# Kernel optimization log

Hardware: AMD Instinct MI355X
Metric: run time of the kernel (lower is better)

Reference implementation:

```python
import jax, jax.numpy as jnp
import numpy as np

B, S, D, I = 4, 2048, 4096, 11008

def setup_inputs() -> dict:
    key = jax.random.key(0)
    ks = jax.random.split(key, 7)
    x = jax.random.normal(ks[0], (B, S, D), dtype=jnp.float32)
    # int8 weights stored as int32 carriers with int8-range values
    gate_w = jax.random.randint(ks[1], (I, D), -127, 128, dtype=jnp.int32)
    up_w = jax.random.randint(ks[2], (I, D), -127, 128, dtype=jnp.int32)
    down_w = jax.random.randint(ks[3], (D, I), -127, 128, dtype=jnp.int32)
    # per-tensor scales (fp16 in original; fp32 here for a clean baseline)
    gate_s = jax.random.uniform(ks[4], (1,), dtype=jnp.float32) * 0.01 + 0.001
    up_s = jax.random.uniform(ks[5], (1,), dtype=jnp.float32) * 0.01 + 0.001
    down_s = jax.random.uniform(ks[6], (1,), dtype=jnp.float32) * 0.01 + 0.001
    return {"x": x, "gate_w": gate_w, "gate_s": gate_s,
            "up_w": up_w, "up_s": up_s, "down_w": down_w, "down_s": down_s}

def _dequant_matmul(x, w_int8, scale):
    # y = x @ (w * s)^T == (x @ w^T) * s  (per-tensor scale commutes)
    w = w_int8.astype(x.dtype)
    return jnp.einsum('bsd,od->bso', x, w) * scale

def reference(x, gate_w, gate_s, up_w, up_s, down_w, down_s):
    gate = jax.nn.silu(_dequant_matmul(x, gate_w, gate_s))  # [B,S,I]
    up = _dequant_matmul(x, up_w, up_s)                      # [B,S,I]
    out = _dequant_matmul(gate * up, down_w, down_s)         # [B,S,D]
    return out.astype(x.dtype)
```

## Files before the change

kernel.cpp:

```cpp
#include <hip/hip_runtime.h>
#include <hip/hip_fp16.h>

#define MTOK 8192
#define DDIM 4096
#define IDIM 11008

#define BM 256
#define BN 128
#define BK 64
#define NTHR 512

typedef _Float16 f16x4 __attribute__((ext_vector_type(4)));
typedef _Float16 f16x8 __attribute__((ext_vector_type(8)));
typedef float    f32x4 __attribute__((ext_vector_type(4)));

__global__ __launch_bounds__(256) void cvt_x_kernel(const float* __restrict__ src,
                                                    _Float16* __restrict__ dst, int n4) {
  int stride = gridDim.x * blockDim.x;
  for (int i = blockIdx.x * blockDim.x + threadIdx.x; i < n4; i += stride) {
    float4 v = ((const float4*)src)[i];
    f16x4 h;
    h.x = (_Float16)v.x; h.y = (_Float16)v.y; h.z = (_Float16)v.z; h.w = (_Float16)v.w;
    ((f16x4*)dst)[i] = h;
  }
}

__global__ __launch_bounds__(256) void cvt_w_kernel(const int* __restrict__ src,
                                                    _Float16* __restrict__ dst, int n4) {
  int stride = gridDim.x * blockDim.x;
  for (int i = blockIdx.x * blockDim.x + threadIdx.x; i < n4; i += stride) {
    int4 v = ((const int4*)src)[i];
    f16x4 h;
    h.x = (_Float16)v.x; h.y = (_Float16)v.y; h.z = (_Float16)v.z; h.w = (_Float16)v.w;
    ((f16x4*)dst)[i] = h;
  }
}

template<int ROWS>
__device__ __forceinline__ void stage_tile(const _Float16* __restrict__ gbase, int ldk,
                                           _Float16* stile, int tid) {
#pragma unroll
  for (int it = 0; it < (ROWS * 8) / NTHR; ++it) {
    int slot = it * NTHR + tid;
    int r = slot >> 3, c = slot & 7;
    int csrc = c ^ (r & 7);
    const _Float16* gp = gbase + (long)r * ldk + csrc * 8;
    __builtin_amdgcn_global_load_lds(
        (const __attribute__((address_space(1))) void*)gp,
        (__attribute__((address_space(3))) void*)(stile + slot * 8),
        16, 0, 0);
  }
}

__device__ __forceinline__ f16x8 frag_ld(const _Float16* s, int row, int cbase) {
  int c = cbase ^ (row & 7);
  return *(const f16x8*)(s + (row * 8 + c) * 8);
}

__global__ __launch_bounds__(NTHR, 2) void gemm_gateup(
    const _Float16* __restrict__ X, const _Float16* __restrict__ Wg,
    const _Float16* __restrict__ Wu, const float* __restrict__ gs_p,
    const float* __restrict__ us_p, _Float16* __restrict__ H) {
  constexpr int ASZ = BM * BK;
  constexpr int BSZ = BN * BK;
  constexpr int BUF = ASZ + 2 * BSZ;
  __shared__ _Float16 lds[2 * BUF] __attribute__((aligned(16)));

  int tid = threadIdx.x;
  int bm = blockIdx.x, bn = blockIdx.y;
  int lane = tid & 63, w = tid >> 6;
  int wm = (w >> 1) * 64, wn = (w & 1) * 64;
  int lr = lane & 15, q = lane >> 4;

  const _Float16* Abase = X + (long)bm * BM * DDIM;
  const _Float16* Gbase = Wg + (long)bn * BN * DDIM;
  const _Float16* Ubase = Wu + (long)bn * BN * DDIM;

  f32x4 accg[4][4], accu[4][4];
#pragma unroll
  for (int i = 0; i < 4; ++i)
#pragma unroll
    for (int j = 0; j < 4; ++j) {
      accg[i][j] = (f32x4){0.f, 0.f, 0.f, 0.f};
      accu[i][j] = (f32x4){0.f, 0.f, 0.f, 0.f};
    }

  stage_tile<BM>(Abase, DDIM, lds, tid);
  stage_tile<BN>(Gbase, DDIM, lds + ASZ, tid);
  stage_tile<BN>(Ubase, DDIM, lds + ASZ + BSZ, tid);
  asm volatile("s_waitcnt vmcnt(0)" ::: "memory");
  __builtin_amdgcn_s_barrier();

  constexpr int NT = DDIM / BK;
#pragma unroll 1
  for (int t = 0; t < NT; ++t) {
    _Float16* cb = lds + (t & 1) * BUF;
    if (t + 1 < NT) {
      _Float16* nb = lds + ((t + 1) & 1) * BUF;
      int k0 = (t + 1) * BK;
      stage_tile<BM>(Abase + k0, DDIM, nb, tid);
      stage_tile<BN>(Gbase + k0, DDIM, nb + ASZ, tid);
      stage_tile<BN>(Ubase + k0, DDIM, nb + ASZ + BSZ, tid);
    }
#pragma unroll
    for (int kk = 0; kk < 2; ++kk) {
      int cbase = kk * 4 + q;
      f16x8 a[4], bg[4], bu[4];
#pragma unroll
      for (int i = 0; i < 4; ++i) a[i] = frag_ld(cb, wm + i * 16 + lr, cbase);
#pragma unroll
      for (int j = 0; j < 4; ++j) {
        bg[j] = frag_ld(cb + ASZ, wn + j * 16 + lr, cbase);
        bu[j] = frag_ld(cb + ASZ + BSZ, wn + j * 16 + lr, cbase);
      }
#pragma unroll
      for (int i = 0; i < 4; ++i)
#pragma unroll
        for (int j = 0; j < 4; ++j) {
          accg[i][j] = __builtin_amdgcn_mfma_f32_16x16x32_f16(a[i], bg[j], accg[i][j], 0, 0, 0);
          accu[i][j] = __builtin_amdgcn_mfma_f32_16x16x32_f16(a[i], bu[j], accu[i][j], 0, 0, 0);
        }
    }
    asm volatile("s_waitcnt vmcnt(0)" ::: "memory");
    __builtin_amdgcn_s_barrier();
  }

  float gs = gs_p[0], us = us_p[0];
#pragma unroll
  for (int i = 0; i < 4; ++i)
#pragma unroll
    for (int j = 0; j < 4; ++j)
#pragma unroll
      for (int r = 0; r < 4; ++r) {
        long m = (long)bm * BM + wm + i * 16 + q * 4 + r;
        long n = (long)bn * BN + wn + j * 16 + lr;
        float g = accg[i][j][r] * gs;
        float u = accu[i][j][r] * us;
        float sg = g / (1.0f + __expf(-g));
        H[m * IDIM + n] = (_Float16)(sg * u * 0.00390625f);
      }
}

__global__ __launch_bounds__(NTHR, 2) void gemm_down(
    const _Float16* __restrict__ Hin, const _Float16* __restrict__ Wd,
    const float* __restrict__ ds_p, float* __restrict__ Out) {
  constexpr int ASZ = BM * BK;
  constexpr int BSZ = BN * BK;
  constexpr int BUF = ASZ + 2 * BSZ;
  __shared__ _Float16 lds[2 * BUF] __attribute__((aligned(16)));

  int tid = threadIdx.x;
  int bm = blockIdx.x, bn = blockIdx.y;
  int lane = tid & 63, w = tid >> 6;
  int wm = (w >> 1) * 64, wn = (w & 1) * 64;
  int lr = lane & 15, q = lane >> 4;

  const _Float16* Abase  = Hin + (long)bm * BM * IDIM;
  const _Float16* B0base = Wd + (long)(bn * 256) * IDIM;
  const _Float16* B1base = Wd + (long)(bn * 256 + 128) * IDIM;

  f32x4 acc0[4][4], acc1[4][4];
#pragma unroll
  for (int i = 0; i < 4; ++i)
#pragma unroll
    for (int j = 0; j < 4; ++j) {
      acc0[i][j] = (f32x4){0.f, 0.f, 0.f, 0.f};
      acc1[i][j] = (f32x4){0.f, 0.f, 0.f, 0.f};
    }

  stage_tile<BM>(Abase, IDIM, lds, tid);
  stage_tile<BN>(B0base, IDIM, lds + ASZ, tid);
  stage_tile<BN>(B1base, IDIM, lds + ASZ + BSZ, tid);
  asm volatile("s_waitcnt vmcnt(0)" ::: "memory");
  __builtin_amdgcn_s_barrier();

  constexpr int NT = IDIM / BK;
#pragma unroll 1
  for (int t = 0; t < NT; ++t) {
    _Float16* cb = lds + (t & 1) * BUF;
    if (t + 1 < NT) {
      _Float16* nb = lds + ((t + 1) & 1) * BUF;
      int k0 = (t + 1) * BK;
      stage_tile<BM>(Abase + k0, IDIM, nb, tid);
      stage_tile<BN>(B0base + k0, IDIM, nb + ASZ, tid);
      stage_tile<BN>(B1base + k0, IDIM, nb + ASZ + BSZ, tid);
    }
#pragma unroll
    for (int kk = 0; kk < 2; ++kk) {
      int cbase = kk * 4 + q;
      f16x8 a[4], b0[4], b1[4];
#pragma unroll
      for (int i = 0; i < 4; ++i) a[i] = frag_ld(cb, wm + i * 16 + lr, cbase);
#pragma unroll
      for (int j = 0; j < 4; ++j) {
        b0[j] = frag_ld(cb + ASZ, wn + j * 16 + lr, cbase);
        b1[j] = frag_ld(cb + ASZ + BSZ, wn + j * 16 + lr, cbase);
      }
#pragma unroll
      for (int i = 0; i < 4; ++i)
#pragma unroll
        for (int j = 0; j < 4; ++j) {
          acc0[i][j] = __builtin_amdgcn_mfma_f32_16x16x32_f16(a[i], b0[j], acc0[i][j], 0, 0, 0);
          acc1[i][j] = __builtin_amdgcn_mfma_f32_16x16x32_f16(a[i], b1[j], acc1[i][j], 0, 0, 0);
        }
    }
    asm volatile("s_waitcnt vmcnt(0)" ::: "memory");
    __builtin_amdgcn_s_barrier();
  }

  float scale = ds_p[0] * 256.0f;
#pragma unroll
  for (int i = 0; i < 4; ++i)
#pragma unroll
    for (int j = 0; j < 4; ++j)
#pragma unroll
      for (int r = 0; r < 4; ++r) {
        long m = (long)bm * BM + wm + i * 16 + q * 4 + r;
        long n = (long)bn * 256 + wn + j * 16 + lr;
        Out[m * DDIM + n] = acc0[i][j][r] * scale;
        Out[m * DDIM + n + 128] = acc1[i][j][r] * scale;
      }
}

extern "C" void kernel_launch(void* const* d_in, const int* in_sizes, int n_in,
                              void* d_out, int out_size, void* d_ws, size_t ws_size,
                              hipStream_t stream) {
  const float* x  = (const float*)d_in[0];
  const int*   gw = (const int*)d_in[1];
  const float* gs = (const float*)d_in[2];
  const int*   uw = (const int*)d_in[3];
  const float* us = (const float*)d_in[4];
  const int*   dw = (const int*)d_in[5];
  const float* ds = (const float*)d_in[6];
  float* out = (float*)d_out;

  char* ws = (char*)d_ws;
  _Float16* xf  = (_Float16*)(ws);
  _Float16* gwf = (_Float16*)(ws + 67108864L);
  _Float16* uwf = (_Float16*)(ws + 157286400L);
  _Float16* dwf = (_Float16*)(ws + 247463936L);
  _Float16* h   = (_Float16*)(ws + 337641472L);

  cvt_x_kernel<<<2048, 256, 0, stream>>>(x, xf, (MTOK * DDIM) / 4);
  cvt_w_kernel<<<2048, 256, 0, stream>>>(gw, gwf, (IDIM * DDIM) / 4);
  cvt_w_kernel<<<2048, 256, 0, stream>>>(uw, uwf, (IDIM * DDIM) / 4);
  cvt_w_kernel<<<2048, 256, 0, stream>>>(dw, dwf, (DDIM * IDIM) / 4);

  dim3 g1(MTOK / BM, IDIM / BN);
  gemm_gateup<<<g1, NTHR, 0, stream>>>(xf, gwf, uwf, gs, us, h);

  dim3 g2(MTOK / BM, DDIM / 256);
  gemm_down<<<g2, NTHR, 0, stream>>>(h, dwf, ds, out);
}
```

Measured before the change: 2.386 ms.

## Use a 4-stage LDS pipeline with BK=32 and an XCD-aware block swizzle

Halves the K tile to 32 and replaces the double buffer with four LDS buffers, so three stages of async global-to-LDS loads stay in flight. A partial vmcnt wait replaces the full drain each iteration. Both GEMMs also remap block IDs so that consecutive tiles land on the same XCD, which should improve L2 reuse. Total LDS footprint is unchanged, but there are twice as many barriers per K and a shallower compute chunk per barrier.

```diff
diff --git a/kernel.cpp b/kernel.cpp
--- a/kernel.cpp
+++ b/kernel.cpp
@@ -7,7 +7,7 @@
 
 #define BM 256
 #define BN 128
-#define BK 64
+#define BK 32
 #define NTHR 512
 
 typedef _Float16 f16x4 __attribute__((ext_vector_type(4)));
@@ -40,10 +40,10 @@
 __device__ __forceinline__ void stage_tile(const _Float16* __restrict__ gbase, int ldk,
                                            _Float16* stile, int tid) {
 #pragma unroll
-  for (int it = 0; it < (ROWS * 8) / NTHR; ++it) {
+  for (int it = 0; it < (ROWS * 4) / NTHR; ++it) {
     int slot = it * NTHR + tid;
-    int r = slot >> 3, c = slot & 7;
-    int csrc = c ^ (r & 7);
+    int r = slot >> 2, c = slot & 3;
+    int csrc = c ^ (r & 3);
     const _Float16* gp = gbase + (long)r * ldk + csrc * 8;
     __builtin_amdgcn_global_load_lds(
         (const __attribute__((address_space(1))) void*)gp,
@@ -53,8 +53,17 @@
 }
 
 __device__ __forceinline__ f16x8 frag_ld(const _Float16* s, int row, int cbase) {
-  int c = cbase ^ (row & 7);
-  return *(const f16x8*)(s + (row * 8 + c) * 8);
+  int c = cbase ^ (row & 3);
+  return *(const f16x8*)(s + (row * 4 + c) * 8);
+}
+
+__device__ __forceinline__ void xcd_swizzle(int& bm, int& bn) {
+  int nwg = gridDim.x * gridDim.y;
+  int lid = blockIdx.y * gridDim.x + blockIdx.x;
+  int cpx = nwg >> 3;
+  int swz = (lid & 7) * cpx + (lid >> 3);
+  bm = swz & (gridDim.x - 1);
+  bn = swz / gridDim.x;
 }
 
 __global__ __launch_bounds__(NTHR, 2) void gemm_gateup(
@@ -64,10 +73,11 @@
   constexpr int ASZ = BM * BK;
   constexpr int BSZ = BN * BK;
   constexpr int BUF = ASZ + 2 * BSZ;
-  __shared__ _Float16 lds[2 * BUF] __attribute__((aligned(16)));
+  __shared__ _Float16 lds[4 * BUF] __attribute__((aligned(16)));
 
   int tid = threadIdx.x;
-  int bm = blockIdx.x, bn = blockIdx.y;
+  int bm, bn;
+  xcd_swizzle(bm, bn);
   int lane = tid & 63, w = tid >> 6;
   int wm = (w >> 1) * 64, wn = (w & 1) * 64;
   int lr = lane & 15, q = lane >> 4;
@@ -85,43 +95,44 @@
       accu[i][j] = (f32x4){0.f, 0.f, 0.f, 0.f};
     }
 
-  stage_tile<BM>(Abase, DDIM, lds, tid);
-  stage_tile<BN>(Gbase, DDIM, lds + ASZ, tid);
-  stage_tile<BN>(Ubase, DDIM, lds + ASZ + BSZ, tid);
-  asm volatile("s_waitcnt vmcnt(0)" ::: "memory");
+  auto stage_all = [&](int s) {
+    _Float16* nb = lds + (s & 3) * BUF;
+    int k0 = s * BK;
+    stage_tile<BM>(Abase + k0, DDIM, nb, tid);
+    stage_tile<BN>(Gbase + k0, DDIM, nb + ASZ, tid);
+    stage_tile<BN>(Ubase + k0, DDIM, nb + ASZ + BSZ, tid);
+  };
+
+  auto compute = [&](const _Float16* cb) {
+    f16x8 a[4], bg[4], bu[4];
+#pragma unroll
+    for (int i = 0; i < 4; ++i) a[i] = frag_ld(cb, wm + i * 16 + lr, q);
+#pragma unroll
+    for (int j = 0; j < 4; ++j) {
+      bg[j] = frag_ld(cb + ASZ, wn + j * 16 + lr, q);
+      bu[j] = frag_ld(cb + ASZ + BSZ, wn + j * 16 + lr, q);
+    }
+#pragma unroll
+    for (int i = 0; i < 4; ++i)
+#pragma unroll
+      for (int j = 0; j < 4; ++j) {
+        accg[i][j] = __builtin_amdgcn_mfma_f32_16x16x32_f16(a[i], bg[j], accg[i][j], 0, 0, 0);
+        accu[i][j] = __builtin_amdgcn_mfma_f32_16x16x32_f16(a[i], bu[j], accu[i][j], 0, 0, 0);
+      }
+  };
+
+  constexpr int NT = DDIM / BK;
+  stage_all(0); stage_all(1); stage_all(2);
+  asm volatile("s_waitcnt vmcnt(8)" ::: "memory");
   __builtin_amdgcn_s_barrier();
 
-  constexpr int NT = DDIM / BK;
 #pragma unroll 1
   for (int t = 0; t < NT; ++t) {
-    _Float16* cb = lds + (t & 1) * BUF;
-    if (t + 1 < NT) {
-      _Float16* nb = lds + ((t + 1) & 1) * BUF;
-      int k0 = (t + 1) * BK;
-      stage_tile<BM>(Abase + k0, DDIM, nb, tid);
-      stage_tile<BN>(Gbase + k0, DDIM, nb + ASZ, tid);
-      stage_tile<BN>(Ubase + k0, DDIM, nb + ASZ + BSZ, tid);
-    }
-#pragma unroll
-    for (int kk = 0; kk < 2; ++kk) {
-      int cbase = kk * 4 + q;
-      f16x8 a[4], bg[4], bu[4];
-#pragma unroll
-      for (int i = 0; i < 4; ++i) a[i] = frag_ld(cb, wm + i * 16 + lr, cbase);
-#pragma unroll
-      for (int j = 0; j < 4; ++j) {
-        bg[j] = frag_ld(cb + ASZ, wn + j * 16 + lr, cbase);
-        bu[j] = frag_ld(cb + ASZ + BSZ, wn + j * 16 + lr, cbase);
-      }
-#pragma unroll
-      for (int i = 0; i < 4; ++i)
-#pragma unroll
-        for (int j = 0; j < 4; ++j) {
-          accg[i][j] = __builtin_amdgcn_mfma_f32_16x16x32_f16(a[i], bg[j], accg[i][j], 0, 0, 0);
-          accu[i][j] = __builtin_amdgcn_mfma_f32_16x16x32_f16(a[i], bu[j], accu[i][j], 0, 0, 0);
-        }
-    }
-    asm volatile("s_waitcnt vmcnt(0)" ::: "memory");
+    if (t + 3 < NT) stage_all(t + 3);
+    compute(lds + (t & 3) * BUF);
+    if (t + 3 < NT)      asm volatile("s_waitcnt vmcnt(8)" ::: "memory");
+    else if (t + 2 < NT) asm volatile("s_waitcnt vmcnt(4)" ::: "memory");
+    else                 asm volatile("s_waitcnt vmcnt(0)" ::: "memory");
     __builtin_amdgcn_s_barrier();
   }
 
@@ -147,10 +158,11 @@
   constexpr int ASZ = BM * BK;
   constexpr int BSZ = BN * BK;
   constexpr int BUF = ASZ + 2 * BSZ;
-  __shared__ _Float16 lds[2 * BUF] __attribute__((aligned(16)));
+  __shared__ _Float16 lds[4 * BUF] __attribute__((aligned(16)));
 
   int tid = threadIdx.x;
-  int bm = blockIdx.x, bn = blockIdx.y;
+  int bm, bn;
+  xcd_swizzle(bm, bn);
   int lane = tid & 63, w = tid >> 6;
   int wm = (w >> 1) * 64, wn = (w & 1) * 64;
   int lr = lane & 15, q = lane >> 4;
@@ -168,43 +180,44 @@
       acc1[i][j] = (f32x4){0.f, 0.f, 0.f, 0.f};
     }
 
-  stage_tile<BM>(Abase, IDIM, lds, tid);
-  stage_tile<BN>(B0base, IDIM, lds + ASZ, tid);
-  stage_tile<BN>(B1base, IDIM, lds + ASZ + BSZ, tid);
-  asm volatile("s_waitcnt vmcnt(0)" ::: "memory");
+  auto stage_all = [&](int s) {
+    _Float16* nb = lds + (s & 3) * BUF;
+    int k0 = s * BK;
+    stage_tile<BM>(Abase + k0, IDIM, nb, tid);
+    stage_tile<BN>(B0base + k0, IDIM, nb + ASZ, tid);
+    stage_tile<BN>(B1base + k0, IDIM, nb + ASZ + BSZ, tid);
+  };
+
+  auto compute = [&](const _Float16* cb) {
+    f16x8 a[4], b0[4], b1[4];
+#pragma unroll
+    for (int i = 0; i < 4; ++i) a[i] = frag_ld(cb, wm + i * 16 + lr, q);
+#pragma unroll
+    for (int j = 0; j < 4; ++j) {
+      b0[j] = frag_ld(cb + ASZ, wn + j * 16 + lr, q);
+      b1[j] = frag_ld(cb + ASZ + BSZ, wn + j * 16 + lr, q);
+    }
+#pragma unroll
+    for (int i = 0; i < 4; ++i)
+#pragma unroll
+      for (int j = 0; j < 4; ++j) {
+        acc0[i][j] = __builtin_amdgcn_mfma_f32_16x16x32_f16(a[i], b0[j], acc0[i][j], 0, 0, 0);
+        acc1[i][j] = __builtin_amdgcn_mfma_f32_16x16x32_f16(a[i], b1[j], acc1[i][j], 0, 0, 0);
+      }
+  };
+
+  constexpr int NT = IDIM / BK;
+  stage_all(0); stage_all(1); stage_all(2);
+  asm volatile("s_waitcnt vmcnt(8)" ::: "memory");
   __builtin_amdgcn_s_barrier();
 
-  constexpr int NT = IDIM / BK;
 #pragma unroll 1
   for (int t = 0; t < NT; ++t) {
-    _Float16* cb = lds + (t & 1) * BUF;
-    if (t + 1 < NT) {
-      _Float16* nb = lds + ((t + 1) & 1) * BUF;
-      int k0 = (t + 1) * BK;
-      stage_tile<BM>(Abase + k0, IDIM, nb, tid);
-      stage_tile<BN>(B0base + k0, IDIM, nb + ASZ, tid);
-      stage_tile<BN>(B1base + k0, IDIM, nb + ASZ + BSZ, tid);
-    }
-#pragma unroll
-    for (int kk = 0; kk < 2; ++kk) {
-      int cbase = kk * 4 + q;
-      f16x8 a[4], b0[4], b1[4];
-#pragma unroll
-      for (int i = 0; i < 4; ++i) a[i] = frag_ld(cb, wm + i * 16 + lr, cbase);
-#pragma unroll
-      for (int j = 0; j < 4; ++j) {
-        b0[j] = frag_ld(cb + ASZ, wn + j * 16 + lr, cbase);
-        b1[j] = frag_ld(cb + ASZ + BSZ, wn + j * 16 + lr, cbase);
-      }
-#pragma unroll
-      for (int i = 0; i < 4; ++i)
-#pragma unroll
-        for (int j = 0; j < 4; ++j) {
-          acc0[i][j] = __builtin_amdgcn_mfma_f32_16x16x32_f16(a[i], b0[j], acc0[i][j], 0, 0, 0);
-          acc1[i][j] = __builtin_amdgcn_mfma_f32_16x16x32_f16(a[i], b1[j], acc1[i][j], 0, 0, 0);
-        }
-    }
-    asm volatile("s_waitcnt vmcnt(0)" ::: "memory");
+    if (t + 3 < NT) stage_all(t + 3);
+    compute(lds + (t & 3) * BUF);
+    if (t + 3 < NT)      asm volatile("s_waitcnt vmcnt(8)" ::: "memory");
+    else if (t + 2 < NT) asm volatile("s_waitcnt vmcnt(4)" ::: "memory");
+    else                 asm volatile("s_waitcnt vmcnt(0)" ::: "memory");
     __builtin_amdgcn_s_barrier();
   }
 
```

Result: slower. 2.842 ms (+19.1%).
